# Optimization experiments

Measured on AMD Instinct MI355X. Metric: run time of the kernel, lower is better.

The kernel has to match this reference:

```python
import jax, jax.numpy as jnp
import numpy as np

BATCH = 4096
IN_FEATURES = 8192
OUT_FEATURES = 8192
N_GROUPS = 1024  # non-overlapping value ranges partitioning [-4, 4]


def setup_inputs() -> dict:
    key = jax.random.key(0)
    k1, k2, k3 = jax.random.split(key, 3)
    x = jax.random.normal(k1, (BATCH, IN_FEATURES), dtype=jnp.float32)
    # Range index metadata (sorted by min, non-overlapping, as _build_range_index assumes)
    edges = jnp.linspace(-4.0, 4.0, N_GROUPS + 1).astype(jnp.float32)
    mins = edges[:-1]
    maxs = edges[1:]
    # Each group owns a full IN_FEATURES-wide weight row in the flat NVMe buffer
    start_pos = jnp.zeros((N_GROUPS,), dtype=jnp.int32)
    sizes = jnp.full((N_GROUPS,), IN_FEATURES, dtype=jnp.int32)
    offsets = (jnp.arange(N_GROUPS, dtype=jnp.int32) * IN_FEATURES)
    weights_flat = jax.random.normal(k2, (N_GROUPS * IN_FEATURES,), dtype=jnp.float32) * 0.02
    # Which output neurons have any metadata entry (others are skipped -> stay 0)
    out_mask = jax.random.randint(k3, (OUT_FEATURES,), 0, 2) > 0
    return {"x": x, "weights_flat": weights_flat, "mins": mins, "maxs": maxs,
            "start_pos": start_pos, "offsets": offsets, "sizes": sizes, "out_mask": out_mask}


def reference(x, weights_flat, mins, maxs, start_pos, offsets, sizes, out_mask):
    B, IN = x.shape
    OUT = out_mask.shape[0]
    G = mins.shape[0]
    # input_val per position: x[:, i].mean() (equals x[0, i] when B == 1)
    val = jnp.mean(x, axis=0)  # [IN]
    # binary search over sorted non-overlapping [min, max] ranges
    g = jnp.searchsorted(mins, val, side='right').astype(jnp.int32) - 1  # [IN]
    gc = jnp.clip(g, 0, G - 1)
    hit = (g >= 0) & (val >= mins[gc]) & (val <= maxs[gc])
    # weight lookup: pos_in_group = in_idx - start_pos, bounds-checked
    pos = jnp.arange(IN, dtype=jnp.int32) - start_pos[gc]
    pos_ok = (pos >= 0) & (pos < sizes[gc])
    idx = jnp.clip(offsets[gc] + pos, 0, weights_flat.shape[0] - 1)
    w = jnp.where(hit & pos_ok, weights_flat[idx], jnp.float32(0))
    # inner MAC loop is independent of out_idx -> same scalar for every covered neuron
    s = jnp.sum(val * w)
    row0 = jnp.where(out_mask, s, jnp.float32(0))  # [OUT]
    out = jnp.zeros((B, OUT), dtype=x.dtype).at[0].set(row0)
    return out
```

## Files before the change

### kernel.cpp

```cpp
#include <hip/hip_runtime.h>

#define BATCH 4096
#define IN_F 8192
#define OUT_F 8192
#define NG 1024
#define NW (NG * IN_F)
#define RCHUNKS 256
#define ROWS_PER_BLK 16


__global__ __launch_bounds__(256) void colsum_kernel(const float* __restrict__ x,
                                                     float4* __restrict__ part4) {
    const int col4 = blockIdx.x * 256 + threadIdx.x;
    const int y = blockIdx.y;
    const float4* __restrict__ xp = (const float4*)x;
    const int stride4 = IN_F / 4;
    long long base = (long long)(y * ROWS_PER_BLK) * stride4 + col4;
    float4 v[ROWS_PER_BLK];
#pragma unroll
    for (int r = 0; r < ROWS_PER_BLK; ++r)
        v[r] = xp[base + (long long)r * stride4];
    float a0 = 0.f, a1 = 0.f, a2 = 0.f, a3 = 0.f;
#pragma unroll
    for (int r = 0; r < ROWS_PER_BLK; ++r) {
        a0 += v[r].x; a1 += v[r].y; a2 += v[r].z; a3 += v[r].w;
    }
    part4[(long long)y * stride4 + col4] = make_float4(a0, a1, a2, a3);
}

__global__ __launch_bounds__(256) void scalar_kernel(const float* __restrict__ part,
                                                     const float* __restrict__ mins,
                                                     const float* __restrict__ maxs,
                                                     const int* __restrict__ start_pos,
                                                     const int* __restrict__ offsets,
                                                     const int* __restrict__ sizes,
                                                     const float* __restrict__ wflat,
                                                     const unsigned char* __restrict__ mask_raw,
                                                     float* __restrict__ spart,
                                                     int* __restrict__ flag) {
    __shared__ float smins[NG];
    __shared__ int sstart[NG];
    __shared__ int soffs[NG];
    __shared__ int ssize[NG];
    __shared__ float sred[256];
    const int t = threadIdx.x;
    for (int i = t; i < NG; i += 256) {
        smins[i]  = mins[i];
        sstart[i] = start_pos[i];
        soffs[i]  = offsets[i];
        ssize[i]  = sizes[i];
    }
    __syncthreads();

    const int j = blockIdx.x * 256 + t;
    float csum = 0.f;
#pragma unroll 8
    for (int y = 0; y < RCHUNKS; ++y)
        csum += part[(long long)y * IN_F + j];
    float val = csum * (1.0f / (float)BATCH);

    int lo = 0, hi = NG;
    while (lo < hi) {
        int mid = (lo + hi) >> 1;
        if (smins[mid] <= val) lo = mid + 1; else hi = mid;
    }
    int g = lo - 1;
    float local = 0.f;
    if (g >= 0 && val >= smins[g] && val <= maxs[g]) {
        int pos = j - sstart[g];
        if (pos >= 0 && pos < ssize[g]) {
            long long idx = (long long)soffs[g] + (long long)pos;
            if (idx < 0) idx = 0;
            if (idx > (long long)(NW - 1)) idx = NW - 1;
            local = val * wflat[idx];
        }
    }
    sred[t] = local;
    __syncthreads();
    for (int ofs = 128; ofs > 0; ofs >>= 1) {
        if (t < ofs) sred[t] += sred[t + ofs];
        __syncthreads();
    }
    if (t == 0) spart[blockIdx.x] = sred[0];

    if (blockIdx.x == 0) {
        const int* mi = (const int*)mask_raw;
        int ok = 1;
#pragma unroll
        for (int i = 0; i < 8; ++i) {
            int v = mi[t * 8 + i];
            ok &= (v == 0 || v == 1) ? 1 : 0;
        }
        __shared__ int sflag[256];
        sflag[t] = ok;
        __syncthreads();
        for (int ofs = 128; ofs > 0; ofs >>= 1) {
            if (t < ofs) sflag[t] &= sflag[t + ofs];
            __syncthreads();
        }
        if (t == 0) *flag = sflag[0];
    }
}

__global__ __launch_bounds__(256) void out_kernel(const unsigned char* __restrict__ mask_raw,
                                                  const float* __restrict__ spart,
                                                  const int* __restrict__ flag,
                                                  float4* __restrict__ out4) {
    const long long total4 = (long long)BATCH * OUT_F / 4;
    const long long stride = (long long)gridDim.x * blockDim.x;
    long long i = (long long)blockIdx.x * blockDim.x + threadIdx.x;
    for (; i < total4; i += stride) {
        float4 v = make_float4(0.f, 0.f, 0.f, 0.f);
        if (i < OUT_F / 4) {
            const float4* sp4 = (const float4*)spart;
            float4 p0 = sp4[0], p1 = sp4[1], p2 = sp4[2], p3 = sp4[3];
            float4 p4 = sp4[4], p5 = sp4[5], p6 = sp4[6], p7 = sp4[7];
            float s = ((p0.x + p0.y + p0.z + p0.w) + (p1.x + p1.y + p1.z + p1.w))
                    + ((p2.x + p2.y + p2.z + p2.w) + (p3.x + p3.y + p3.z + p3.w))
                    + ((p4.x + p4.y + p4.z + p4.w) + (p5.x + p5.y + p5.z + p5.w))
                    + ((p6.x + p6.y + p6.z + p6.w) + (p7.x + p7.y + p7.z + p7.w));
            const int mask_is_i32 = *flag;
            const int j = (int)i * 4;
            int m0, m1, m2, m3;
            if (mask_is_i32) {
                const int* mi = (const int*)mask_raw;
                m0 = mi[j]; m1 = mi[j + 1]; m2 = mi[j + 2]; m3 = mi[j + 3];
            } else {
                m0 = mask_raw[j]; m1 = mask_raw[j + 1];
                m2 = mask_raw[j + 2]; m3 = mask_raw[j + 3];
            }
            v.x = m0 ? s : 0.f; v.y = m1 ? s : 0.f;
            v.z = m2 ? s : 0.f; v.w = m3 ? s : 0.f;
        }
        out4[i] = v;
    }
}

extern "C" void kernel_launch(void* const* d_in, const int* in_sizes, int n_in,
                              void* d_out, int out_size, void* d_ws, size_t ws_size,
                              hipStream_t stream) {
    const float* x          = (const float*)d_in[0];
    const float* wflat      = (const float*)d_in[1];
    const float* mins       = (const float*)d_in[2];
    const float* maxs       = (const float*)d_in[3];
    const int*   start_pos  = (const int*)d_in[4];
    const int*   offsets    = (const int*)d_in[5];
    const int*   sizes      = (const int*)d_in[6];
    const unsigned char* mask = (const unsigned char*)d_in[7];

    float* part   = (float*)d_ws;
    float* spart  = part + (long long)RCHUNKS * IN_F;
    int*   flag   = (int*)(spart + 32);

    colsum_kernel<<<dim3(IN_F / (256 * 4), RCHUNKS), 256, 0, stream>>>(x, (float4*)part);
    scalar_kernel<<<IN_F / 256, 256, 0, stream>>>(part, mins, maxs, start_pos, offsets,
                                                  sizes, wflat, mask, spart, flag);
    out_kernel<<<2048, 256, 0, stream>>>(mask, spart, flag, (float4*)d_out);
}
```

Baseline: 275.0 us.

## Fuse output zeroing into colsum kernel and shrink final kernel to row 0

Moves the zero-fill of output rows 1..B-1 into the column-sum kernel using nontemporal stores, so the 128MB output write overlaps with the 128MB read of x instead of running as a separate kernel after the scalar reduction. The final kernel now writes only row 0. The scalar kernel also batches 64 loads per iteration to raise memory-level parallelism. The cost is that colsum now carries both read and write traffic, plus more register pressure in scalar_kernel.

```diff
diff --git a/kernel.cpp b/kernel.cpp
--- a/kernel.cpp
+++ b/kernel.cpp
@@ -8,9 +8,12 @@
 #define RCHUNKS 256
 #define ROWS_PER_BLK 16
 
+typedef float f4raw __attribute__((ext_vector_type(4)));
 
-__global__ __launch_bounds__(256) void colsum_kernel(const float* __restrict__ x,
-                                                     float4* __restrict__ part4) {
+
+__global__ __launch_bounds__(256) void colsum_zero_kernel(const float* __restrict__ x,
+                                                          float4* __restrict__ part4,
+                                                          float4* __restrict__ out4) {
     const int col4 = blockIdx.x * 256 + threadIdx.x;
     const int y = blockIdx.y;
     const float4* __restrict__ xp = (const float4*)x;
@@ -20,6 +23,21 @@
 #pragma unroll
     for (int r = 0; r < ROWS_PER_BLK; ++r)
         v[r] = xp[base + (long long)r * stride4];
+
+    {
+        const long long lin = ((long long)blockIdx.y * gridDim.x + blockIdx.x) * 256
+                            + threadIdx.x;
+        const long long nthreads = 524288;
+        const f4raw z = (f4raw){0.f, 0.f, 0.f, 0.f};
+        f4raw* __restrict__ outr = (f4raw*)out4;
+#pragma unroll
+        for (int k = 0; k < 16; ++k) {
+            long long idx = (long long)(OUT_F / 4) + lin + (long long)k * nthreads;
+            if (idx < (long long)BATCH * OUT_F / 4)
+                __builtin_nontemporal_store(z, &outr[idx]);
+        }
+    }
+
     float a0 = 0.f, a1 = 0.f, a2 = 0.f, a3 = 0.f;
 #pragma unroll
     for (int r = 0; r < ROWS_PER_BLK; ++r) {
@@ -54,9 +72,17 @@
 
     const int j = blockIdx.x * 256 + t;
     float csum = 0.f;
-#pragma unroll 8
-    for (int y = 0; y < RCHUNKS; ++y)
-        csum += part[(long long)y * IN_F + j];
+    const float* __restrict__ pj = part + j;
+#pragma unroll 1
+    for (int y0 = 0; y0 < RCHUNKS; y0 += 64) {
+        float v[64];
+#pragma unroll
+        for (int i = 0; i < 64; ++i)
+            v[i] = pj[(long long)(y0 + i) * IN_F];
+#pragma unroll
+        for (int i = 0; i < 64; ++i)
+            csum += v[i];
+    }
     float val = csum * (1.0f / (float)BATCH);
 
     int lo = 0, hi = NG;
@@ -102,38 +128,30 @@
     }
 }
 
-__global__ __launch_bounds__(256) void out_kernel(const unsigned char* __restrict__ mask_raw,
-                                                  const float* __restrict__ spart,
-                                                  const int* __restrict__ flag,
-                                                  float4* __restrict__ out4) {
-    const long long total4 = (long long)BATCH * OUT_F / 4;
-    const long long stride = (long long)gridDim.x * blockDim.x;
-    long long i = (long long)blockIdx.x * blockDim.x + threadIdx.x;
-    for (; i < total4; i += stride) {
-        float4 v = make_float4(0.f, 0.f, 0.f, 0.f);
-        if (i < OUT_F / 4) {
-            const float4* sp4 = (const float4*)spart;
-            float4 p0 = sp4[0], p1 = sp4[1], p2 = sp4[2], p3 = sp4[3];
-            float4 p4 = sp4[4], p5 = sp4[5], p6 = sp4[6], p7 = sp4[7];
-            float s = ((p0.x + p0.y + p0.z + p0.w) + (p1.x + p1.y + p1.z + p1.w))
-                    + ((p2.x + p2.y + p2.z + p2.w) + (p3.x + p3.y + p3.z + p3.w))
-                    + ((p4.x + p4.y + p4.z + p4.w) + (p5.x + p5.y + p5.z + p5.w))
-                    + ((p6.x + p6.y + p6.z + p6.w) + (p7.x + p7.y + p7.z + p7.w));
-            const int mask_is_i32 = *flag;
-            const int j = (int)i * 4;
-            int m0, m1, m2, m3;
-            if (mask_is_i32) {
-                const int* mi = (const int*)mask_raw;
-                m0 = mi[j]; m1 = mi[j + 1]; m2 = mi[j + 2]; m3 = mi[j + 3];
-            } else {
-                m0 = mask_raw[j]; m1 = mask_raw[j + 1];
-                m2 = mask_raw[j + 2]; m3 = mask_raw[j + 3];
-            }
-            v.x = m0 ? s : 0.f; v.y = m1 ? s : 0.f;
-            v.z = m2 ? s : 0.f; v.w = m3 ? s : 0.f;
-        }
-        out4[i] = v;
+__global__ __launch_bounds__(256) void row0_kernel(const unsigned char* __restrict__ mask_raw,
+                                                   const float* __restrict__ spart,
+                                                   const int* __restrict__ flag,
+                                                   float4* __restrict__ out4) {
+    const int i = blockIdx.x * 256 + threadIdx.x;
+    const float4* sp4 = (const float4*)spart;
+    float4 p0 = sp4[0], p1 = sp4[1], p2 = sp4[2], p3 = sp4[3];
+    float4 p4 = sp4[4], p5 = sp4[5], p6 = sp4[6], p7 = sp4[7];
+    float s = ((p0.x + p0.y + p0.z + p0.w) + (p1.x + p1.y + p1.z + p1.w))
+            + ((p2.x + p2.y + p2.z + p2.w) + (p3.x + p3.y + p3.z + p3.w))
+            + ((p4.x + p4.y + p4.z + p4.w) + (p5.x + p5.y + p5.z + p5.w))
+            + ((p6.x + p6.y + p6.z + p6.w) + (p7.x + p7.y + p7.z + p7.w));
+    const int mask_is_i32 = *flag;
+    const int j = i * 4;
+    int m0, m1, m2, m3;
+    if (mask_is_i32) {
+        const int* mi = (const int*)mask_raw;
+        m0 = mi[j]; m1 = mi[j + 1]; m2 = mi[j + 2]; m3 = mi[j + 3];
+    } else {
+        m0 = mask_raw[j]; m1 = mask_raw[j + 1];
+        m2 = mask_raw[j + 2]; m3 = mask_raw[j + 3];
     }
+    float4 v = make_float4(m0 ? s : 0.f, m1 ? s : 0.f, m2 ? s : 0.f, m3 ? s : 0.f);
+    out4[i] = v;
 }
 
 extern "C" void kernel_launch(void* const* d_in, const int* in_sizes, int n_in,
@@ -152,8 +170,9 @@
     float* spart  = part + (long long)RCHUNKS * IN_F;
     int*   flag   = (int*)(spart + 32);
 
-    colsum_kernel<<<dim3(IN_F / (256 * 4), RCHUNKS), 256, 0, stream>>>(x, (float4*)part);
+    colsum_zero_kernel<<<dim3(IN_F / (256 * 4), RCHUNKS), 256, 0, stream>>>(
+        x, (float4*)part, (float4*)d_out);
     scalar_kernel<<<IN_F / 256, 256, 0, stream>>>(part, mins, maxs, start_pos, offsets,
                                                   sizes, wflat, mask, spart, flag);
-    out_kernel<<<2048, 256, 0, stream>>>(mask, spart, flag, (float4*)d_out);
+    row0_kernel<<<OUT_F / (256 * 4), 256, 0, stream>>>(mask, spart, flag, (float4*)d_out);
 }
```

New measurement: 269.4 us. 1.02x faster.
